# Optimization experiments

Measured on AMD Instinct MI355X. Metric: run time of the kernel, lower is better.

The kernel has to match this reference:

```python
import jax, jax.numpy as jnp
import numpy as np

NEG_BIG = 1e8  # mask value from the original code


def setup_inputs() -> dict:
    key = jax.random.key(0)
    k1, k2, k3, k4, k5 = jax.random.split(key, 5)
    B, L, H, D = 16, 128, 256, 256
    # xavier-uniform-ish scale for the weight matrices
    lim = float(np.sqrt(6.0 / (H + D)))
    return {
        "encoder_output": jax.random.normal(k1, (B, L, H), dtype=jnp.float32),
        "W_l": jax.random.uniform(k2, (H, D), jnp.float32, -lim, lim),
        "W_r": jax.random.uniform(k3, (H, D), jnp.float32, -lim, lim),
        "U": jax.random.uniform(k4, (D,), jnp.float32, 0.0, 1.0),
        "logit_bias": jax.random.uniform(k5, (1,), jnp.float32, 0.0, 1.0),
    }


def reference(encoder_output, W_l, W_r, U, logit_bias):
    B, L, H = encoder_output.shape
    # projections: (B, L, D)
    dot_l = jnp.einsum("blh,hd->bld", encoder_output, W_l)
    dot_r = jnp.einsum("blh,hd->bld", encoder_output, W_r)
    # pairwise additive attention: (B, L, L, D) -> (B, L, L)
    final_sum = jnp.tanh(dot_l[:, :, None, :] + dot_r[:, None, :, :])
    logits = jnp.einsum("bijd,d->bij", final_sum, U) + logit_bias[0]
    # per-step diagonal mask (one_hot(i) at step i) vectorized as eye
    mask = jnp.eye(L, dtype=logits.dtype)  # (L, L)
    mask_scores = logits - NEG_BIG * mask[None, :, :]  # (B, L, L)
    probs = jax.nn.sigmoid(mask_scores)
    # Bernoulli sample (fixed key for reproducibility)
    samples = jax.random.bernoulli(jax.random.key(1), probs).astype(logits.dtype)  # graphs (B,L,L)
    # Bernoulli entropy: p*softplus(-l) + (1-p)*softplus(l), numerically stable
    entropy = probs * jax.nn.softplus(-mask_scores) + (1.0 - probs) * jax.nn.softplus(mask_scores)
    graph_batch = jnp.mean(samples, axis=0)  # (L, L)
    # BCE-with-logits mean over all elements (targets = sampled graphs)
    log_softmax = jnp.mean(jax.nn.softplus(mask_scores) - mask_scores * samples)
    entropy_regularization = jnp.mean(jnp.mean(entropy, axis=2), axis=1)  # (B,)
    return (mask_scores, samples, entropy, graph_batch, log_softmax, entropy_regularization)
```

## Files before the change

kernel.cpp:

```cpp
#include <hip/hip_runtime.h>

#define Bn 16
#define Ln 128
#define Hn 256
#define Dn 256

#define OFF_MASK   0
#define OFF_SMP    262144
#define OFF_ENT    524288
#define OFF_GRAPH  786432
#define OFF_LSE    802816
#define OFF_EREG   802817

static __device__ __forceinline__ unsigned rotl32(unsigned x, int r) {
  return (x << r) | (x >> (32 - r));
}

static __device__ __forceinline__ unsigned threefry_bits(unsigned c_hi, unsigned c_lo) {
  const unsigned ks0 = 0u, ks1 = 1u;
  const unsigned ks2 = 0u ^ 1u ^ 0x1BD11BDAu;
  unsigned x0 = c_hi + ks0;
  unsigned x1 = c_lo + ks1;
  x0 += x1; x1 = rotl32(x1, 13); x1 ^= x0;
  x0 += x1; x1 = rotl32(x1, 15); x1 ^= x0;
  x0 += x1; x1 = rotl32(x1, 26); x1 ^= x0;
  x0 += x1; x1 = rotl32(x1, 6);  x1 ^= x0;
  x0 += ks1; x1 += ks2 + 1u;
  x0 += x1; x1 = rotl32(x1, 17); x1 ^= x0;
  x0 += x1; x1 = rotl32(x1, 29); x1 ^= x0;
  x0 += x1; x1 = rotl32(x1, 16); x1 ^= x0;
  x0 += x1; x1 = rotl32(x1, 24); x1 ^= x0;
  x0 += ks2; x1 += ks0 + 2u;
  x0 += x1; x1 = rotl32(x1, 13); x1 ^= x0;
  x0 += x1; x1 = rotl32(x1, 15); x1 ^= x0;
  x0 += x1; x1 = rotl32(x1, 26); x1 ^= x0;
  x0 += x1; x1 = rotl32(x1, 6);  x1 ^= x0;
  x0 += ks0; x1 += ks1 + 3u;
  x0 += x1; x1 = rotl32(x1, 17); x1 ^= x0;
  x0 += x1; x1 = rotl32(x1, 29); x1 ^= x0;
  x0 += x1; x1 = rotl32(x1, 16); x1 ^= x0;
  x0 += x1; x1 = rotl32(x1, 24); x1 ^= x0;
  x0 += ks1; x1 += ks2 + 4u;
  x0 += x1; x1 = rotl32(x1, 13); x1 ^= x0;
  x0 += x1; x1 = rotl32(x1, 15); x1 ^= x0;
  x0 += x1; x1 = rotl32(x1, 26); x1 ^= x0;
  x0 += x1; x1 = rotl32(x1, 6);  x1 ^= x0;
  x0 += ks2; x1 += ks0 + 5u;
  return x0 ^ x1;
}

static __device__ __forceinline__ float softplus_f(float x) {
  return fmaxf(x, 0.0f) + log1pf(__expf(-fabsf(x)));
}

static __device__ __forceinline__ float fast_tanh(float x) {
  float e = __expf(-2.0f * x);
  float r = __builtin_amdgcn_rcpf(1.0f + e);
  return fmaf(2.0f, r, -1.0f);
}

__global__ void proj_kernel(const float* __restrict__ enc,
                            const float* __restrict__ Wl,
                            const float* __restrict__ Wr,
                            float* __restrict__ dl,
                            float* __restrict__ dr,
                            float* __restrict__ out,
                            double* __restrict__ ws_acc) {
  int gid = blockIdx.x * blockDim.x + threadIdx.x;
  if (gid < Ln * Ln) out[OFF_GRAPH + gid] = 0.0f;
  if (gid < 18) ws_acc[gid] = 0.0;

  int g = blockIdx.x;
  int rg = g >> 3;
  int mat = (g >> 2) & 1;
  int dq = g & 3;
  int r0 = rg * 16;
  int d0 = dq * 64;

  int t = threadIdx.x;
  int dcol = d0 + (t & 63);
  int rsub = t >> 6;

  __shared__ float encS[16][Hn];
#pragma unroll
  for (int q = 0; q < 4; ++q)
    ((float4*)encS)[q * 256 + t] = ((const float4*)(enc + (size_t)r0 * Hn))[q * 256 + t];
  __syncthreads();

  const float* wp = (mat ? Wr : Wl) + dcol;
  float a[4] = {0.f, 0.f, 0.f, 0.f};

  for (int h8 = 0; h8 < Hn / 8; ++h8) {
    float wv[8];
#pragma unroll
    for (int u = 0; u < 8; ++u) wv[u] = wp[(size_t)(h8 * 8 + u) * Dn];
#pragma unroll
    for (int u = 0; u < 8; ++u) {
      int h = h8 * 8 + u;
#pragma unroll
      for (int rr = 0; rr < 4; ++rr)
        a[rr] = fmaf(encS[rsub * 4 + rr][h], wv[u], a[rr]);
    }
  }

  float* dst = mat ? dr : dl;
#pragma unroll
  for (int rr = 0; rr < 4; ++rr)
    dst[(size_t)(r0 + rsub * 4 + rr) * Dn + dcol] = a[rr];
}

__global__ void pair_kernel(const float* __restrict__ dl,
                            const float* __restrict__ dr,
                            const float* __restrict__ U,
                            const float* __restrict__ bias,
                            float* __restrict__ out,
                            double* __restrict__ ws_acc) {
  int blk = blockIdx.x;
  int b = blk >> 6;
  int i0 = ((blk >> 1) & 31) * 4;
  int j0 = (blk & 1) * 64;
  int t = threadIdx.x;
  int dp = t & 15;
  int jj = t >> 4;

  __shared__ float dlS[4][Dn];
  __shared__ float pS[4][64 * 17];
  __shared__ float redS[8];

  ((float4*)dlS)[t] = ((const float4*)(dl + (size_t)(b * Ln + i0) * Dn))[t];

  float Ur[16];
  {
    const float4* U4 = (const float4*)(U + dp * 16);
#pragma unroll
    for (int q = 0; q < 4; ++q) {
      float4 u = U4[q];
      Ur[4*q+0] = u.x; Ur[4*q+1] = u.y; Ur[4*q+2] = u.z; Ur[4*q+3] = u.w;
    }
  }
  __syncthreads();

  float dlr[4][16];
#pragma unroll
  for (int r = 0; r < 4; ++r) {
#pragma unroll
    for (int q = 0; q < 4; ++q) {
      float4 a = *(const float4*)&dlS[r][dp * 16 + q * 4];
      dlr[r][4*q+0] = a.x; dlr[r][4*q+1] = a.y; dlr[r][4*q+2] = a.z; dlr[r][4*q+3] = a.w;
    }
  }

  const float* drt = dr + (size_t)b * Ln * Dn + (size_t)(j0 + jj) * Dn + dp * 16;
#pragma unroll
  for (int tl = 0; tl < 4; ++tl) {
    const float4* drp = (const float4*)(drt + (size_t)tl * 16 * Dn);
    float a0 = 0.f, a1 = 0.f, a2 = 0.f, a3 = 0.f;
#pragma unroll
    for (int q = 0; q < 4; ++q) {
      float4 v = drp[q];
#pragma unroll
      for (int c = 0; c < 4; ++c) {
        float dv = (c == 0) ? v.x : (c == 1) ? v.y : (c == 2) ? v.z : v.w;
        float uv = Ur[4*q+c];
        a0 = fmaf(fast_tanh(dlr[0][4*q+c] + dv), uv, a0);
        a1 = fmaf(fast_tanh(dlr[1][4*q+c] + dv), uv, a1);
        a2 = fmaf(fast_tanh(dlr[2][4*q+c] + dv), uv, a2);
        a3 = fmaf(fast_tanh(dlr[3][4*q+c] + dv), uv, a3);
      }
    }
    int sa = (tl * 16 + jj) * 17 + dp;
    pS[0][sa] = a0; pS[1][sa] = a1; pS[2][sa] = a2; pS[3][sa] = a3;
  }
  __syncthreads();

  int row = t >> 6;
  int jl = t & 63;
  int j = j0 + jl;
  const float* ps = &pS[row][jl * 17];
  float tot = 0.0f;
#pragma unroll
  for (int k = 0; k < 16; ++k) tot += ps[k];
  int i = i0 + row;
  float l = tot + bias[0] - ((j == i) ? 1.0e8f : 0.0f);
  float e = __expf(-l);
  float p = __builtin_amdgcn_rcpf(1.0f + e);
  unsigned n = ((unsigned)(b * Ln + i) << 7) | (unsigned)j;
  unsigned bits = threefry_bits(0u, n);
  float u = __uint_as_float((bits >> 9) | 0x3f800000u) - 1.0f;
  float smp = (u < p) ? 1.0f : 0.0f;
  float sp_pos = softplus_f(l);
  float sp_neg = softplus_f(-l);
  float ent = p * sp_neg + (1.0f - p) * sp_pos;
  size_t idx = (size_t)(b * Ln + i) * Ln + j;
  out[OFF_MASK + idx] = l;
  out[OFF_SMP + idx] = smp;
  out[OFF_ENT + idx] = ent;
  atomicAdd(&out[OFF_GRAPH + i * Ln + j], smp * 0.0625f);
  float ent_v = ent;
  float lse_v = sp_pos - l * smp;

#pragma unroll
  for (int off = 32; off > 0; off >>= 1) {
    ent_v += __shfl_down(ent_v, off);
    lse_v += __shfl_down(lse_v, off);
  }
  if ((t & 63) == 0) {
    redS[(t >> 6) * 2 + 0] = ent_v;
    redS[(t >> 6) * 2 + 1] = lse_v;
  }
  __syncthreads();
  if (t == 0) {
    float es = redS[0] + redS[2] + redS[4] + redS[6];
    float ls = redS[1] + redS[3] + redS[5] + redS[7];
    atomicAdd(&ws_acc[b], (double)es);
    atomicAdd(&ws_acc[16], (double)ls);
    __threadfence();
    unsigned int* ctr = (unsigned int*)&ws_acc[17];
    unsigned done = atomicAdd(ctr, 1u);
    if (done == (unsigned)(gridDim.x - 1)) {
      double ls_tot = atomicAdd(&ws_acc[16], 0.0);
      out[OFF_LSE] = (float)(ls_tot / (double)(Bn * Ln * Ln));
      for (int q = 0; q < Bn; ++q) {
        double ev = atomicAdd(&ws_acc[q], 0.0);
        out[OFF_EREG + q] = (float)(ev / (double)(Ln * Ln));
      }
    }
  }
}

extern "C" void kernel_launch(void* const* d_in, const int* in_sizes, int n_in,
                              void* d_out, int out_size, void* d_ws, size_t ws_size,
                              hipStream_t stream) {
  const float* enc = (const float*)d_in[0];
  const float* Wl = (const float*)d_in[1];
  const float* Wr = (const float*)d_in[2];
  const float* U = (const float*)d_in[3];
  const float* bias = (const float*)d_in[4];
  float* out = (float*)d_out;

  float* dl = (float*)d_ws;
  float* dr = dl + (size_t)Bn * Ln * Dn;
  double* ws_acc = (double*)(dr + (size_t)Bn * Ln * Dn);

  proj_kernel<<<1024, 256, 0, stream>>>(enc, Wl, Wr, dl, dr, out, ws_acc);
  pair_kernel<<<Bn * Ln / 2, 256, 0, stream>>>(dl, dr, U, bias, out, ws_acc);
}
```

Before: 125.3 us.

## Retile projection GEMM with float4 weights and prefetch dr rows in pair kernel

The projection kernel is retiled so each block covers 8 rows and the full 256-wide D of one matrix. Each thread computes 2 rows by 4 columns using float4 weight loads and reads the encoder values directly from global memory (wave-uniform via readfirstlane) instead of staging them in shared memory. The grid drops from 1024 to 512 blocks. The pair kernel gains launch bounds and double-buffers the dr loads across its four tile iterations so memory latency overlaps the tanh work, at the cost of extra registers.

```diff
diff --git a/kernel.cpp b/kernel.cpp
--- a/kernel.cpp
+++ b/kernel.cpp
@@ -59,7 +59,8 @@
   return fmaf(2.0f, r, -1.0f);
 }
 
-__global__ void proj_kernel(const float* __restrict__ enc,
+__global__ __launch_bounds__(256) void proj_kernel(
+                            const float* __restrict__ enc,
                             const float* __restrict__ Wl,
                             const float* __restrict__ Wr,
                             float* __restrict__ dl,
@@ -71,45 +72,51 @@
   if (gid < 18) ws_acc[gid] = 0.0;
 
   int g = blockIdx.x;
-  int rg = g >> 3;
-  int mat = (g >> 2) & 1;
-  int dq = g & 3;
-  int r0 = rg * 16;
-  int d0 = dq * 64;
+  int rg = g >> 1;
+  int mat = g & 1;
+  int r0 = rg * 8;
 
   int t = threadIdx.x;
-  int dcol = d0 + (t & 63);
+  int d4 = (t & 63) * 4;
   int rsub = t >> 6;
 
-  __shared__ float encS[16][Hn];
-#pragma unroll
-  for (int q = 0; q < 4; ++q)
-    ((float4*)encS)[q * 256 + t] = ((const float4*)(enc + (size_t)r0 * Hn))[q * 256 + t];
-  __syncthreads();
-
-  const float* wp = (mat ? Wr : Wl) + dcol;
-  float a[4] = {0.f, 0.f, 0.f, 0.f};
-
+  int row0 = __builtin_amdgcn_readfirstlane(r0 + rsub * 2);
+  const float* ep0 = enc + (size_t)row0 * Hn;
+  const float* ep1 = ep0 + Hn;
+  const float* wbase = (mat ? Wr : Wl) + d4;
+
+  float4 a0 = {0.f, 0.f, 0.f, 0.f};
+  float4 a1 = {0.f, 0.f, 0.f, 0.f};
+
+#pragma unroll 2
   for (int h8 = 0; h8 < Hn / 8; ++h8) {
-    float wv[8];
-#pragma unroll
-    for (int u = 0; u < 8; ++u) wv[u] = wp[(size_t)(h8 * 8 + u) * Dn];
+    float4 w[8];
+#pragma unroll
+    for (int u = 0; u < 8; ++u)
+      w[u] = *(const float4*)(wbase + (size_t)(h8 * 8 + u) * Dn);
 #pragma unroll
     for (int u = 0; u < 8; ++u) {
       int h = h8 * 8 + u;
-#pragma unroll
-      for (int rr = 0; rr < 4; ++rr)
-        a[rr] = fmaf(encS[rsub * 4 + rr][h], wv[u], a[rr]);
-    }
-  }
-
-  float* dst = mat ? dr : dl;
-#pragma unroll
-  for (int rr = 0; rr < 4; ++rr)
-    dst[(size_t)(r0 + rsub * 4 + rr) * Dn + dcol] = a[rr];
-}
-
-__global__ void pair_kernel(const float* __restrict__ dl,
+      float e0 = ep0[h];
+      float e1 = ep1[h];
+      a0.x = fmaf(e0, w[u].x, a0.x);
+      a0.y = fmaf(e0, w[u].y, a0.y);
+      a0.z = fmaf(e0, w[u].z, a0.z);
+      a0.w = fmaf(e0, w[u].w, a0.w);
+      a1.x = fmaf(e1, w[u].x, a1.x);
+      a1.y = fmaf(e1, w[u].y, a1.y);
+      a1.z = fmaf(e1, w[u].z, a1.z);
+      a1.w = fmaf(e1, w[u].w, a1.w);
+    }
+  }
+
+  float* dst = (mat ? dr : dl) + (size_t)(r0 + rsub * 2) * Dn + d4;
+  *(float4*)dst = a0;
+  *(float4*)(dst + Dn) = a1;
+}
+
+__global__ __launch_bounds__(256, 4) void pair_kernel(
+                            const float* __restrict__ dl,
                             const float* __restrict__ dr,
                             const float* __restrict__ U,
                             const float* __restrict__ bias,
@@ -151,13 +158,23 @@
   }
 
   const float* drt = dr + (size_t)b * Ln * Dn + (size_t)(j0 + jj) * Dn + dp * 16;
+  float4 vbuf[2][4];
+  {
+    const float4* drp = (const float4*)drt;
+#pragma unroll
+    for (int q = 0; q < 4; ++q) vbuf[0][q] = drp[q];
+  }
 #pragma unroll
   for (int tl = 0; tl < 4; ++tl) {
-    const float4* drp = (const float4*)(drt + (size_t)tl * 16 * Dn);
+    if (tl < 3) {
+      const float4* drn = (const float4*)(drt + (size_t)(tl + 1) * 16 * Dn);
+#pragma unroll
+      for (int q = 0; q < 4; ++q) vbuf[(tl + 1) & 1][q] = drn[q];
+    }
     float a0 = 0.f, a1 = 0.f, a2 = 0.f, a3 = 0.f;
 #pragma unroll
     for (int q = 0; q < 4; ++q) {
-      float4 v = drp[q];
+      float4 v = vbuf[tl & 1][q];
 #pragma unroll
       for (int c = 0; c < 4; ++c) {
         float dv = (c == 0) ? v.x : (c == 1) ? v.y : (c == 2) ? v.z : v.w;
@@ -242,6 +259,6 @@
   float* dr = dl + (size_t)Bn * Ln * Dn;
   double* ws_acc = (double*)(dr + (size_t)Bn * Ln * Dn);
 
-  proj_kernel<<<1024, 256, 0, stream>>>(enc, Wl, Wr, dl, dr, out, ws_acc);
+  proj_kernel<<<512, 256, 0, stream>>>(enc, Wl, Wr, dl, dr, out, ws_acc);
   pair_kernel<<<Bn * Ln / 2, 256, 0, stream>>>(dl, dr, U, bias, out, ws_acc);
 }
```

Measured after the change: 124.2 us. No clear change (-0.9%).
